# Optimization experiments

Measured on AMD Instinct MI355X. Metric: run time of the kernel, lower is better.

The kernel has to match this reference:

```python
import jax
import jax.numpy as jnp
import numpy as np

NV, NH, COND_DIM, HW = 256, 256, 16, 64
B = 8192
T_END = 1.0
T_START = 5.0
FALLOFF = 0.1


def setup_inputs() -> dict:
    key = jax.random.key(0)
    ks = jax.random.split(key, 4)
    return {
        "cond": jax.random.normal(ks[0], (B, COND_DIM), dtype=jnp.float32),
        "W": jax.random.normal(ks[1], (NV, NH), dtype=jnp.float32) * 0.01,
        "b": jnp.zeros((NV,), jnp.float32),
        "c": jnp.zeros((NH,), jnp.float32),
        "fc1_w": jax.random.normal(ks[2], (HW, COND_DIM), dtype=jnp.float32) * (1.0 / np.sqrt(COND_DIM)),
        "fc1_b": jnp.zeros((HW,), jnp.float32),
        "fc2_w": jax.random.normal(ks[3], (2 * (NV + NH), HW), dtype=jnp.float32) * (1.0 / np.sqrt(HW)),
        "fc2_b": jnp.zeros((2 * (NV + NH),), jnp.float32),
        "steps": 32,
    }


def reference(cond, W, b, c, fc1_w, fc1_b, fc2_w, fc2_b, steps):
    nv, nh = W.shape
    # Conditioner: torch Linear convention y = x @ W.T + b
    x = jnp.tanh(cond @ fc1_w.T + fc1_b)
    x = x @ fc2_w.T + fc2_b  # [B, 2*(nv+nh)]
    gamma_b, beta_b, gamma_c, beta_c = jnp.split(x, [nv, 2 * nv, 2 * nv + nh], axis=-1)
    b_mod = (1.0 + gamma_b) * b + beta_b  # [B, nv]
    c_mod = (1.0 + gamma_c) * c + beta_c  # [B, nh]

    batch = cond.shape[0]
    key = jax.random.key(42)
    key, k0 = jax.random.split(key)
    v = jax.random.bernoulli(k0, 0.5, (batch, nv)).astype(W.dtype)
    s0 = jnp.ones((batch, 1), W.dtype)

    # sigmoid annealing schedule
    t = jnp.arange(steps, dtype=W.dtype)
    s = 1.0 / (1.0 + jnp.exp(FALLOFF * (t - steps / 2.0)))
    temps = T_END + (T_START - T_END) * s  # [steps]

    bsum = jnp.sum(b_mod, axis=-1)  # [B], constant across steps

    def gibbs_step(carry, T):
        v, s0, key = carry
        key, kh, ks0, kv = jax.random.split(key, 4)
        # symmetric flip of visibles
        v_eff = s0 * v + (1.0 - s0) * (1.0 - v)
        p_h = jax.nn.sigmoid((v_eff @ W + c_mod) / T)
        h = jax.random.bernoulli(kh, p_h).astype(v.dtype)  # [B, nh]
        a = h @ W.T  # [B, nv]
        vb = jnp.sum(v * b_mod, axis=-1)
        va = jnp.sum(v * a, axis=-1)
        asum = jnp.sum(a, axis=-1)
        dE = -bsum - asum + 2.0 * vb + 2.0 * va  # [B]
        p_s0 = jax.nn.sigmoid(dE / T)
        s0 = jax.random.bernoulli(ks0, p_s0).astype(v.dtype)[:, None]  # [B,1]
        p_v = jax.nn.sigmoid((a + b_mod) / T)
        v_eff2 = jax.random.bernoulli(kv, p_v).astype(v.dtype)
        v_next = s0 * v_eff2 + (1.0 - s0) * (1.0 - v_eff2)
        return (v_next, s0, key), None

    (v, s0, key), _ = jax.lax.scan(gibbs_step, (v, s0, key), temps)
    return v, temps
```

## Files before the change

kernel.cpp:

```cpp
#include <hip/hip_runtime.h>
#include <math.h>

#pragma clang fp contract(off)

namespace {

constexpr int kSteps = 32;

constexpr size_t OFF_TEMPS = 0;
constexpr size_t OFF_KEYS  = 64;
constexpr size_t OFF_WP    = 512;
constexpr size_t OFF_WTP   = 66048;
constexpr size_t OFF_F2T   = 131584;
constexpr size_t OFF_X1    = 197120;
constexpr size_t OFF_BMOD  = 721408;
constexpr size_t OFF_CMOD  = 2818560;
constexpr size_t WS_FLOATS = 4915712;

__device__ __forceinline__ unsigned rotl32(unsigned v, int n) {
  return (v << n) | (v >> (32 - n));
}

__device__ __forceinline__ void tf_block(unsigned k0, unsigned k1,
                                         unsigned c0, unsigned c1,
                                         unsigned* o0, unsigned* o1) {
  unsigned k2 = k0 ^ k1 ^ 0x1BD11BDAu;
  unsigned x0 = c0 + k0;
  unsigned x1 = c1 + k1;
  x0 += x1; x1 = rotl32(x1, 13); x1 ^= x0;
  x0 += x1; x1 = rotl32(x1, 15); x1 ^= x0;
  x0 += x1; x1 = rotl32(x1, 26); x1 ^= x0;
  x0 += x1; x1 = rotl32(x1, 6);  x1 ^= x0;
  x0 += k1; x1 += k2 + 1u;
  x0 += x1; x1 = rotl32(x1, 17); x1 ^= x0;
  x0 += x1; x1 = rotl32(x1, 29); x1 ^= x0;
  x0 += x1; x1 = rotl32(x1, 16); x1 ^= x0;
  x0 += x1; x1 = rotl32(x1, 24); x1 ^= x0;
  x0 += k2; x1 += k0 + 2u;
  x0 += x1; x1 = rotl32(x1, 13); x1 ^= x0;
  x0 += x1; x1 = rotl32(x1, 15); x1 ^= x0;
  x0 += x1; x1 = rotl32(x1, 26); x1 ^= x0;
  x0 += x1; x1 = rotl32(x1, 6);  x1 ^= x0;
  x0 += k0; x1 += k1 + 3u;
  x0 += x1; x1 = rotl32(x1, 17); x1 ^= x0;
  x0 += x1; x1 = rotl32(x1, 29); x1 ^= x0;
  x0 += x1; x1 = rotl32(x1, 16); x1 ^= x0;
  x0 += x1; x1 = rotl32(x1, 24); x1 ^= x0;
  x0 += k1; x1 += k2 + 4u;
  x0 += x1; x1 = rotl32(x1, 13); x1 ^= x0;
  x0 += x1; x1 = rotl32(x1, 15); x1 ^= x0;
  x0 += x1; x1 = rotl32(x1, 26); x1 ^= x0;
  x0 += x1; x1 = rotl32(x1, 6);  x1 ^= x0;
  x0 += k2; x1 += k0 + 5u;
  *o0 = x0; *o1 = x1;
}

__device__ __forceinline__ float tf_uniform(unsigned k0, unsigned k1, unsigned idx) {
  unsigned o0, o1;
  tf_block(k0, k1, 0u, idx, &o0, &o1);
  unsigned bits = o0 ^ o1;
  float f = __uint_as_float((bits >> 9) | 0x3f800000u);
  return f - 1.0f;
}

__device__ __forceinline__ float xla_tanhf(float x) {
  if (fabsf(x) < 0.0004f) return x;
  float xc = fminf(fmaxf(x, -9.0f), 9.0f);
  float x2 = xc * xc;
  float num = -2.76076847742355e-16f;
  num = num * x2 + 2.00018790482477e-13f;
  num = num * x2 + -8.60467152213735e-11f;
  num = num * x2 + 5.12229709037114e-08f;
  num = num * x2 + 1.48572235717979e-05f;
  num = num * x2 + 6.37261928875436e-04f;
  num = num * x2 + 4.89352455891786e-03f;
  num = xc * num;
  float den = 1.19825839466702e-06f;
  den = den * x2 + 1.18534705686654e-04f;
  den = den * x2 + 2.26843463243900e-03f;
  den = den * x2 + 4.89352518554385e-03f;
  return num / den;
}

__device__ __forceinline__ float xla_sigmoid(float x) {
  return 0.5f + 0.5f * xla_tanhf(0.5f * x);
}

__global__ __launch_bounds__(64) void kInitMeta(float* temps, unsigned* keys) {
  int t = threadIdx.x;
  if (t < 32) {
    float tf = (float)t;
    float arg = 0.1f * (tf - 16.0f);
    float e = (float)exp((double)arg);
    float s = 1.0f / (1.0f + e);
    temps[t] = 1.0f + 4.0f * s;
  }
  if (t == 0) {
    unsigned cur0 = 0u, cur1 = 42u;
    unsigned a0, a1, b0, b1;
    tf_block(cur0, cur1, 0u, 0u, &a0, &a1);
    tf_block(cur0, cur1, 0u, 1u, &b0, &b1);
    keys[0] = b0; keys[1] = b1;
    cur0 = a0; cur1 = a1;
    for (int st = 0; st < kSteps; ++st) {
      unsigned n0, n1, kh0, kh1, ks0a, ks0b, kv0, kv1;
      tf_block(cur0, cur1, 0u, 0u, &n0, &n1);
      tf_block(cur0, cur1, 0u, 1u, &kh0, &kh1);
      tf_block(cur0, cur1, 0u, 2u, &ks0a, &ks0b);
      tf_block(cur0, cur1, 0u, 3u, &kv0, &kv1);
      keys[2 + st * 6 + 0] = kh0;  keys[2 + st * 6 + 1] = kh1;
      keys[2 + st * 6 + 2] = ks0a; keys[2 + st * 6 + 3] = ks0b;
      keys[2 + st * 6 + 4] = kv0;  keys[2 + st * 6 + 5] = kv1;
      cur0 = n0; cur1 = n1;
    }
  }
}

__global__ __launch_bounds__(256) void kWp(const float* __restrict__ W, float4* __restrict__ Wp) {
  int idx = blockIdx.x * 256 + threadIdx.x;
  int kb = idx >> 8, j = idx & 255;
  float4 w;
  w.x = W[(4 * kb + 0) * 256 + j];
  w.y = W[(4 * kb + 1) * 256 + j];
  w.z = W[(4 * kb + 2) * 256 + j];
  w.w = W[(4 * kb + 3) * 256 + j];
  Wp[idx] = w;
}

__global__ __launch_bounds__(256) void kWtp(const float* __restrict__ W, float4* __restrict__ Wtp) {
  int idx = blockIdx.x * 256 + threadIdx.x;
  int kb = idx >> 8, i = idx & 255;
  float4 w;
  w.x = W[i * 256 + 4 * kb + 0];
  w.y = W[i * 256 + 4 * kb + 1];
  w.z = W[i * 256 + 4 * kb + 2];
  w.w = W[i * 256 + 4 * kb + 3];
  Wtp[idx] = w;
}

__global__ __launch_bounds__(256) void kTf2(const float* __restrict__ fc2w, float* __restrict__ fc2wT) {
  int idx = blockIdx.x * 256 + threadIdx.x;
  int k = idx >> 10, o = idx & 1023;
  fc2wT[idx] = fc2w[o * 64 + k];
}

__global__ __launch_bounds__(256) void kX1(const float* __restrict__ cond,
                                           const float* __restrict__ fc1w,
                                           const float* __restrict__ fc1b,
                                           float* __restrict__ x1) {
  int idx = blockIdx.x * 256 + threadIdx.x;
  int b = idx >> 6, hh = idx & 63;
  float acc = 0.0f;
  for (int k = 0; k < 16; ++k)
    acc = acc + cond[b * 16 + k] * fc1w[hh * 16 + k];
  acc = acc + fc1b[hh];
  x1[idx] = xla_tanhf(acc);
}

__global__ __launch_bounds__(256) void kMod2(const float* __restrict__ x1,
                                             const float* __restrict__ fc2wT,
                                             const float* __restrict__ fc2b,
                                             const float* __restrict__ bvec,
                                             const float* __restrict__ cvec,
                                             float* __restrict__ bmod,
                                             float* __restrict__ cmod) {
  const int bid = blockIdx.x;
  const int b = bid >> 1;
  const int half = bid & 1;
  const int ii = threadIdx.x;
  const int og = half * 512 + ii;
  const int ob = og + 256;
  float dg = 0.0f, db = 0.0f;
  for (int k = 0; k < 64; ++k) {
    float xv = x1[b * 64 + k];
    dg = dg + xv * fc2wT[k * 1024 + og];
    db = db + xv * fc2wT[k * 1024 + ob];
  }
  dg = dg + fc2b[og];
  db = db + fc2b[ob];
  float base = half ? cvec[ii] : bvec[ii];
  float outv = (1.0f + dg) * base + db;
  if (half) cmod[b * 256 + ii] = outv;
  else      bmod[b * 256 + ii] = outv;
}

__global__ __launch_bounds__(256, 4) void kGibbs(
    const float4* __restrict__ Wp, const float4* __restrict__ Wtp,
    const float* __restrict__ bmod, const float* __restrict__ cmod,
    const unsigned* __restrict__ keys, const float* __restrict__ temps,
    float* __restrict__ out) {
  __shared__ float4 X4[8][65];
  __shared__ float  vlds[8][257];
  __shared__ float  bmlds[8][257];
  __shared__ float  cmlds[8][257];
  __shared__ float  chainres[8][3];
  __shared__ float  bsum_s[8];
  __shared__ int    s0i[8];

  float* Xf = reinterpret_cast<float*>(X4);

  const int j = threadIdx.x;
  const int brow = blockIdx.x * 8;

#pragma unroll
  for (int r = 0; r < 8; ++r) {
    bmlds[r][j] = bmod[(brow + r) * 256 + j];
    cmlds[r][j] = cmod[(brow + r) * 256 + j];
  }
  if (j < 8) s0i[j] = 1;
  {
    const unsigned k00 = keys[0], k01 = keys[1];
#pragma unroll
    for (int r = 0; r < 8; ++r) {
      float u = tf_uniform(k00, k01, (unsigned)((brow + r) * 256 + j));
      vlds[r][j] = (u < 0.5f) ? 1.0f : 0.0f;
    }
  }
  __syncthreads();
  if (j < 8) {
    float s = 0.0f;
    for (int k = 0; k < 256; ++k) s = s + bmlds[j][k];
    bsum_s[j] = s;
  }

  for (int t = 0; t < kSteps; ++t) {
    const float T = temps[t];
    const unsigned kh0 = keys[2 + t * 6 + 0], kh1 = keys[2 + t * 6 + 1];
    const unsigned ksa = keys[2 + t * 6 + 2], ksb = keys[2 + t * 6 + 3];
    const unsigned kv0 = keys[2 + t * 6 + 4], kv1 = keys[2 + t * 6 + 5];

#pragma unroll
    for (int r = 0; r < 8; ++r) {
      float vv = vlds[r][j];
      Xf[r * 260 + j] = s0i[r] ? vv : 1.0f - vv;
    }
    __syncthreads();

    float acc[8];
#pragma unroll
    for (int r = 0; r < 8; ++r) acc[r] = 0.0f;
    {
      const float4* wp = Wp + j;
      for (int kb = 0; kb < 64; ++kb) {
        float4 w4 = wp[kb << 8];
#pragma unroll
        for (int r = 0; r < 8; ++r) {
          float4 v4 = X4[r][kb];
          acc[r] = __builtin_fmaf(v4.x, w4.x, acc[r]);
          acc[r] = __builtin_fmaf(v4.y, w4.y, acc[r]);
          acc[r] = __builtin_fmaf(v4.z, w4.z, acc[r]);
          acc[r] = __builtin_fmaf(v4.w, w4.w, acc[r]);
        }
      }
    }

    float hv[8];
#pragma unroll
    for (int r = 0; r < 8; ++r) {
      float z = (acc[r] + cmlds[r][j]) / T;
      float p = xla_sigmoid(z);
      float u = tf_uniform(kh0, kh1, (unsigned)((brow + r) * 256 + j));
      hv[r] = (u < p) ? 1.0f : 0.0f;
    }
    __syncthreads();
#pragma unroll
    for (int r = 0; r < 8; ++r) Xf[r * 260 + j] = hv[r];
    __syncthreads();

#pragma unroll
    for (int r = 0; r < 8; ++r) acc[r] = 0.0f;
    {
      const float4* wp = Wtp + j;
      for (int kb = 0; kb < 64; ++kb) {
        float4 w4 = wp[kb << 8];
#pragma unroll
        for (int r = 0; r < 8; ++r) {
          float4 v4 = X4[r][kb];
          acc[r] = __builtin_fmaf(v4.x, w4.x, acc[r]);
          acc[r] = __builtin_fmaf(v4.y, w4.y, acc[r]);
          acc[r] = __builtin_fmaf(v4.z, w4.z, acc[r]);
          acc[r] = __builtin_fmaf(v4.w, w4.w, acc[r]);
        }
      }
    }

    float ve2[8];
#pragma unroll
    for (int r = 0; r < 8; ++r) {
      float z = (acc[r] + bmlds[r][j]) / T;
      float p = xla_sigmoid(z);
      float u = tf_uniform(kv0, kv1, (unsigned)((brow + r) * 256 + j));
      ve2[r] = (u < p) ? 1.0f : 0.0f;
    }

    __syncthreads();
#pragma unroll
    for (int r = 0; r < 8; ++r) Xf[r * 260 + j] = acc[r];
    __syncthreads();

    if (j < 64) {
      if (j < 24) {
        const int r = j / 3, c = j % 3;
        const float* A = &vlds[r][0];
        const float* Y = (c == 0) ? &bmlds[r][0] : &Xf[r * 260];
        float s = 0.0f;
        for (int k = 0; k < 256; ++k) {
          float xm = (c == 2) ? 1.0f : A[k];
          s = __builtin_fmaf(xm, Y[k], s);
        }
        chainres[r][c] = s;
      }
    }
    __syncthreads();

    if (j < 8) {
      const int r = j;
      float vb = chainres[r][0], va = chainres[r][1], as = chainres[r][2];
      float dE = ((-bsum_s[r] - as) + 2.0f * vb) + 2.0f * va;
      float z = dE / T;
      float p = xla_sigmoid(z);
      float u = tf_uniform(ksa, ksb, (unsigned)(brow + r));
      s0i[r] = (u < p) ? 1 : 0;
    }
    __syncthreads();

#pragma unroll
    for (int r = 0; r < 8; ++r) {
      vlds[r][j] = s0i[r] ? ve2[r] : 1.0f - ve2[r];
    }
    __syncthreads();
  }

#pragma unroll
  for (int r = 0; r < 8; ++r)
    out[(brow + r) * 256 + j] = vlds[r][j];
  if (blockIdx.x == 0 && j < 32) out[2097152 + j] = temps[j];
}

}

extern "C" void kernel_launch(void* const* d_in, const int* in_sizes, int n_in,
                              void* d_out, int out_size, void* d_ws, size_t ws_size,
                              hipStream_t stream) {
  (void)in_sizes; (void)n_in; (void)out_size;
  const float* cond = (const float*)d_in[0];
  const float* W    = (const float*)d_in[1];
  const float* bvec = (const float*)d_in[2];
  const float* cvec = (const float*)d_in[3];
  const float* fc1w = (const float*)d_in[4];
  const float* fc1b = (const float*)d_in[5];
  const float* fc2w = (const float*)d_in[6];
  const float* fc2b = (const float*)d_in[7];

  if (ws_size < WS_FLOATS * sizeof(float)) return;

  float* ws      = (float*)d_ws;
  float* temps   = ws + OFF_TEMPS;
  unsigned* keys = (unsigned*)(ws + OFF_KEYS);
  float4* Wp     = (float4*)(ws + OFF_WP);
  float4* Wtp    = (float4*)(ws + OFF_WTP);
  float* fc2wT   = ws + OFF_F2T;
  float* x1      = ws + OFF_X1;
  float* bmod    = ws + OFF_BMOD;
  float* cmod    = ws + OFF_CMOD;
  float* out     = (float*)d_out;

  hipLaunchKernelGGL(kInitMeta, dim3(1), dim3(64), 0, stream, temps, keys);
  hipLaunchKernelGGL(kWp, dim3(256), dim3(256), 0, stream, W, Wp);
  hipLaunchKernelGGL(kWtp, dim3(256), dim3(256), 0, stream, W, Wtp);
  hipLaunchKernelGGL(kTf2, dim3(256), dim3(256), 0, stream, fc2w, fc2wT);
  hipLaunchKernelGGL(kX1, dim3(2048), dim3(256), 0, stream, cond, fc1w, fc1b, x1);
  hipLaunchKernelGGL(kMod2, dim3(16384), dim3(256), 0, stream, x1, fc2wT, fc2b, bvec, cvec, bmod, cmod);
  hipLaunchKernelGGL(kGibbs, dim3(1024), dim3(256), 0, stream, Wp, Wtp, bmod, cmod, keys, temps, out);
}
```

Before: 1.930 ms.

## Halve rows per Gibbs block, keep modulations in registers, drop v_eff pass

```diff
diff --git a/kernel.cpp b/kernel.cpp
--- a/kernel.cpp
+++ b/kernel.cpp
@@ -184,42 +184,48 @@
   else      bmod[b * 256 + ii] = outv;
 }
 
-__global__ __launch_bounds__(256, 4) void kGibbs(
+__global__ __launch_bounds__(256, 6) void kGibbs(
     const float4* __restrict__ Wp, const float4* __restrict__ Wtp,
     const float* __restrict__ bmod, const float* __restrict__ cmod,
     const unsigned* __restrict__ keys, const float* __restrict__ temps,
     float* __restrict__ out) {
-  __shared__ float4 X4[8][65];
-  __shared__ float  vlds[8][257];
-  __shared__ float  bmlds[8][257];
-  __shared__ float  cmlds[8][257];
-  __shared__ float  chainres[8][3];
-  __shared__ float  bsum_s[8];
-  __shared__ int    s0i[8];
-
-  float* Xf = reinterpret_cast<float*>(X4);
+  __shared__ float4 X4[4][65];
+  __shared__ float4 A4[4][65];
+  __shared__ float4 V4[4][65];
+  __shared__ float4 BM4[4][65];
+  __shared__ float  chainres[12];
+  __shared__ float  bsum_s[4];
+  __shared__ int    s0i[4];
+
+  float* Xf  = reinterpret_cast<float*>(X4);
+  float* Af  = reinterpret_cast<float*>(A4);
+  float* Vf  = reinterpret_cast<float*>(V4);
+  float* BMf = reinterpret_cast<float*>(BM4);
 
   const int j = threadIdx.x;
-  const int brow = blockIdx.x * 8;
-
-#pragma unroll
-  for (int r = 0; r < 8; ++r) {
-    bmlds[r][j] = bmod[(brow + r) * 256 + j];
-    cmlds[r][j] = cmod[(brow + r) * 256 + j];
-  }
-  if (j < 8) s0i[j] = 1;
+  const int brow = blockIdx.x * 4;
+
+  float bmv[4], cmv[4];
   {
     const unsigned k00 = keys[0], k01 = keys[1];
 #pragma unroll
-    for (int r = 0; r < 8; ++r) {
-      float u = tf_uniform(k00, k01, (unsigned)((brow + r) * 256 + j));
-      vlds[r][j] = (u < 0.5f) ? 1.0f : 0.0f;
-    }
-  }
+    for (int r = 0; r < 4; ++r) {
+      const int gi = (brow + r) * 256 + j;
+      float bm = bmod[gi];
+      bmv[r] = bm; cmv[r] = cmod[gi];
+      BMf[r * 260 + j] = bm;
+      float u = tf_uniform(k00, k01, (unsigned)gi);
+      float vv = (u < 0.5f) ? 1.0f : 0.0f;
+      Vf[r * 260 + j] = vv;
+      Xf[r * 260 + j] = vv;
+    }
+  }
+  if (j < 4) s0i[j] = 1;
   __syncthreads();
-  if (j < 8) {
+  if (j < 4) {
+    const float* B = BMf + j * 260;
     float s = 0.0f;
-    for (int k = 0; k < 256; ++k) s = s + bmlds[j][k];
+    for (int k = 0; k < 256; ++k) s = s + B[k];
     bsum_s[j] = s;
   }
 
@@ -229,65 +235,58 @@
     const unsigned ksa = keys[2 + t * 6 + 2], ksb = keys[2 + t * 6 + 3];
     const unsigned kv0 = keys[2 + t * 6 + 4], kv1 = keys[2 + t * 6 + 5];
 
-#pragma unroll
-    for (int r = 0; r < 8; ++r) {
-      float vv = vlds[r][j];
-      Xf[r * 260 + j] = s0i[r] ? vv : 1.0f - vv;
-    }
-    __syncthreads();
-
-    float acc[8];
-#pragma unroll
-    for (int r = 0; r < 8; ++r) acc[r] = 0.0f;
+    float acc[4];
+#pragma unroll
+    for (int r = 0; r < 4; ++r) acc[r] = 0.0f;
     {
       const float4* wp = Wp + j;
       for (int kb = 0; kb < 64; ++kb) {
-        float4 w4 = wp[kb << 8];
-#pragma unroll
-        for (int r = 0; r < 8; ++r) {
-          float4 v4 = X4[r][kb];
-          acc[r] = __builtin_fmaf(v4.x, w4.x, acc[r]);
-          acc[r] = __builtin_fmaf(v4.y, w4.y, acc[r]);
-          acc[r] = __builtin_fmaf(v4.z, w4.z, acc[r]);
-          acc[r] = __builtin_fmaf(v4.w, w4.w, acc[r]);
+        float4 w = wp[kb << 8];
+#pragma unroll
+        for (int r = 0; r < 4; ++r) {
+          float4 x = X4[r][kb];
+          acc[r] = __builtin_fmaf(x.x, w.x, acc[r]);
+          acc[r] = __builtin_fmaf(x.y, w.y, acc[r]);
+          acc[r] = __builtin_fmaf(x.z, w.z, acc[r]);
+          acc[r] = __builtin_fmaf(x.w, w.w, acc[r]);
         }
       }
     }
 
-    float hv[8];
-#pragma unroll
-    for (int r = 0; r < 8; ++r) {
-      float z = (acc[r] + cmlds[r][j]) / T;
+    float hv[4];
+#pragma unroll
+    for (int r = 0; r < 4; ++r) {
+      float z = (acc[r] + cmv[r]) / T;
       float p = xla_sigmoid(z);
       float u = tf_uniform(kh0, kh1, (unsigned)((brow + r) * 256 + j));
       hv[r] = (u < p) ? 1.0f : 0.0f;
     }
     __syncthreads();
 #pragma unroll
-    for (int r = 0; r < 8; ++r) Xf[r * 260 + j] = hv[r];
-    __syncthreads();
-
-#pragma unroll
-    for (int r = 0; r < 8; ++r) acc[r] = 0.0f;
+    for (int r = 0; r < 4; ++r) Xf[r * 260 + j] = hv[r];
+    __syncthreads();
+
+#pragma unroll
+    for (int r = 0; r < 4; ++r) acc[r] = 0.0f;
     {
       const float4* wp = Wtp + j;
       for (int kb = 0; kb < 64; ++kb) {
-        float4 w4 = wp[kb << 8];
-#pragma unroll
-        for (int r = 0; r < 8; ++r) {
-          float4 v4 = X4[r][kb];
-          acc[r] = __builtin_fmaf(v4.x, w4.x, acc[r]);
-          acc[r] = __builtin_fmaf(v4.y, w4.y, acc[r]);
-          acc[r] = __builtin_fmaf(v4.z, w4.z, acc[r]);
-          acc[r] = __builtin_fmaf(v4.w, w4.w, acc[r]);
+        float4 w = wp[kb << 8];
+#pragma unroll
+        for (int r = 0; r < 4; ++r) {
+          float4 x = X4[r][kb];
+          acc[r] = __builtin_fmaf(x.x, w.x, acc[r]);
+          acc[r] = __builtin_fmaf(x.y, w.y, acc[r]);
+          acc[r] = __builtin_fmaf(x.z, w.z, acc[r]);
+          acc[r] = __builtin_fmaf(x.w, w.w, acc[r]);
         }
       }
     }
 
-    float ve2[8];
-#pragma unroll
-    for (int r = 0; r < 8; ++r) {
-      float z = (acc[r] + bmlds[r][j]) / T;
+    float ve2[4];
+#pragma unroll
+    for (int r = 0; r < 4; ++r) {
+      float z = (acc[r] + bmv[r]) / T;
       float p = xla_sigmoid(z);
       float u = tf_uniform(kv0, kv1, (unsigned)((brow + r) * 256 + j));
       ve2[r] = (u < p) ? 1.0f : 0.0f;
@@ -295,27 +294,34 @@
 
     __syncthreads();
 #pragma unroll
-    for (int r = 0; r < 8; ++r) Xf[r * 260 + j] = acc[r];
-    __syncthreads();
-
-    if (j < 64) {
-      if (j < 24) {
-        const int r = j / 3, c = j % 3;
-        const float* A = &vlds[r][0];
-        const float* Y = (c == 0) ? &bmlds[r][0] : &Xf[r * 260];
-        float s = 0.0f;
-        for (int k = 0; k < 256; ++k) {
-          float xm = (c == 2) ? 1.0f : A[k];
-          s = __builtin_fmaf(xm, Y[k], s);
-        }
-        chainres[r][c] = s;
+    for (int r = 0; r < 4; ++r) {
+      Af[r * 260 + j] = acc[r];
+      Xf[r * 260 + j] = ve2[r];
+    }
+    __syncthreads();
+
+    if (j < 12) {
+      const int r = j / 3, c = j % 3;
+      const float4* A4c = reinterpret_cast<const float4*>(Vf + r * 260);
+      const float4* Y4c = reinterpret_cast<const float4*>(
+          ((c == 0) ? BMf : Af) + r * 260);
+      const bool isAs = (c == 2);
+      float s = 0.0f;
+      for (int q = 0; q < 64; ++q) {
+        float4 a4 = A4c[q];
+        float4 y4 = Y4c[q];
+        float m0 = isAs ? 1.0f : a4.x; s = __builtin_fmaf(m0, y4.x, s);
+        float m1 = isAs ? 1.0f : a4.y; s = __builtin_fmaf(m1, y4.y, s);
+        float m2 = isAs ? 1.0f : a4.z; s = __builtin_fmaf(m2, y4.z, s);
+        float m3 = isAs ? 1.0f : a4.w; s = __builtin_fmaf(m3, y4.w, s);
       }
-    }
-    __syncthreads();
-
-    if (j < 8) {
+      chainres[j] = s;
+    }
+    __syncthreads();
+
+    if (j < 4) {
       const int r = j;
-      float vb = chainres[r][0], va = chainres[r][1], as = chainres[r][2];
+      float vb = chainres[3 * r], va = chainres[3 * r + 1], as = chainres[3 * r + 2];
       float dE = ((-bsum_s[r] - as) + 2.0f * vb) + 2.0f * va;
       float z = dE / T;
       float p = xla_sigmoid(z);
@@ -325,15 +331,14 @@
     __syncthreads();
 
 #pragma unroll
-    for (int r = 0; r < 8; ++r) {
-      vlds[r][j] = s0i[r] ? ve2[r] : 1.0f - ve2[r];
-    }
-    __syncthreads();
-  }
-
-#pragma unroll
-  for (int r = 0; r < 8; ++r)
-    out[(brow + r) * 256 + j] = vlds[r][j];
+    for (int r = 0; r < 4; ++r) {
+      Vf[r * 260 + j] = s0i[r] ? ve2[r] : 1.0f - ve2[r];
+    }
+  }
+
+#pragma unroll
+  for (int r = 0; r < 4; ++r)
+    out[(brow + r) * 256 + j] = Vf[r * 260 + j];
   if (blockIdx.x == 0 && j < 32) out[2097152 + j] = temps[j];
 }
 
@@ -371,5 +376,5 @@
   hipLaunchKernelGGL(kTf2, dim3(256), dim3(256), 0, stream, fc2w, fc2wT);
   hipLaunchKernelGGL(kX1, dim3(2048), dim3(256), 0, stream, cond, fc1w, fc1b, x1);
   hipLaunchKernelGGL(kMod2, dim3(16384), dim3(256), 0, stream, x1, fc2wT, fc2b, bvec, cvec, bmod, cmod);
-  hipLaunchKernelGGL(kGibbs, dim3(1024), dim3(256), 0, stream, Wp, Wtp, bmod, cmod, keys, temps, out);
-}
+  hipLaunchKernelGGL(kGibbs, dim3(2048), dim3(256), 0, stream, Wp, Wtp, bmod, cmod, keys, temps, out);
+}
```

New measurement: 2.345 ms. 21.5% more time.
